# Kernel tuning notes

Measured on AMD Instinct MI355X. Metric: run time of the kernel, lower is better.

Reference implementation:

```python
import jax, jax.numpy as jnp
import numpy as np
from jax import lax

KSIZE = 33          # spatially-varying kernel is 33x33
PAD = 16            # ReplicationPad2d(16)
THRESH = 0.0001     # taps with weight <= 1e-4 are skipped (treated as zero)


def setup_inputs() -> dict:
    key = jax.random.key(0)
    k1, k2 = jax.random.split(key)
    inputImg = jax.random.uniform(k1, (1, 3, 256, 256), dtype=jnp.float32)
    Kernels = jax.random.uniform(k2, (1, KSIZE * KSIZE, 256, 256), dtype=jnp.float32)
    return {"inputImg": inputImg, "Kernels": Kernels}


def reference(inputImg, Kernels):
    B, C, H, W = inputImg.shape
    # Replication (edge) padding by 16 on both spatial dims
    padded = jnp.pad(inputImg, ((0, 0), (0, 0), (PAD, PAD), (PAD, PAD)), mode="edge")
    # Extract all 33x33 patches: [B, C*1089, H, W], channel-major then (fh, fw)
    patches = lax.conv_general_dilated_patches(
        padded, (KSIZE, KSIZE), (1, 1), "VALID",
        dimension_numbers=("NCHW", "OIHW", "NCHW"))
    patches = patches.reshape(B, C, KSIZE * KSIZE, H, W)
    # Threshold: original loop skips taps with kernel weight <= 1e-4
    Keff = jnp.where(Kernels > THRESH, Kernels, jnp.zeros_like(Kernels))  # [B, 1089, H, W]
    # Per-pixel dynamic convolution: sum over the 1089 taps
    out = jnp.einsum("bckhw,bkhw->bchw", patches, Keff)
    return out
```

## Files before the change

kernel.cpp:

```cpp
#include <hip/hip_runtime.h>

#define IMG_H 256
#define IMG_W 256
#define IMG_C 3
#define KS 33
#define PAD 16
#define THRESH 1e-4f
#define FH_PER 3

__global__ __launch_bounds__(256, 4)
void reblur_kernel(const float* __restrict__ img,
                   const float* __restrict__ ker,
                   float* __restrict__ out)
{
    const int x = threadIdx.x;
    const int y = blockIdx.x;
    const int chunk = blockIdx.y;
    const int fh0 = chunk * FH_PER;

    const int pix = y * IMG_W + x;
    const int plane = IMG_H * IMG_W;

    const float* kp = ker + (size_t)(fh0 * KS) * plane + pix;

    float a0 = 0.f, a1 = 0.f, a2 = 0.f;
    const int xm = x - PAD;

    #pragma unroll
    for (int dfh = 0; dfh < FH_PER; ++dfh) {
        int yy = y + (fh0 + dfh) - PAD;
        yy = yy < 0 ? 0 : (yy > IMG_H - 1 ? IMG_H - 1 : yy);
        const float* __restrict__ r0 = img + yy * IMG_W;
        const float* __restrict__ r1 = r0 + plane;
        const float* __restrict__ r2 = r1 + plane;
        #pragma unroll
        for (int fw = 0; fw < KS; ++fw) {
            float w = *kp;
            kp += plane;
            int xx = xm + fw;
            xx = xx < 0 ? 0 : (xx > IMG_W - 1 ? IMG_W - 1 : xx);
            float we = (w > THRESH) ? w : 0.f;
            a0 = fmaf(we, r0[xx], a0);
            a1 = fmaf(we, r1[xx], a1);
            a2 = fmaf(we, r2[xx], a2);
        }
    }

    atomicAdd(out + pix,             a0);
    atomicAdd(out + plane + pix,     a1);
    atomicAdd(out + 2 * plane + pix, a2);
}

extern "C" void kernel_launch(void* const* d_in, const int* in_sizes, int n_in,
                              void* d_out, int out_size, void* d_ws, size_t ws_size,
                              hipStream_t stream) {
    const float* img = (const float*)d_in[0];
    const float* ker = (const float*)d_in[1];
    float* out = (float*)d_out;

    hipMemsetAsync(out, 0, (size_t)out_size * sizeof(float), stream);

    dim3 grid(IMG_H, (KS + FH_PER - 1) / FH_PER);
    reblur_kernel<<<grid, IMG_W, 0, stream>>>(img, ker, out);
}
```

Baseline: 381.7 us.

## Stage padded image rows in LDS and compute four pixels per thread with float4

```diff
diff --git a/kernel.cpp b/kernel.cpp
--- a/kernel.cpp
+++ b/kernel.cpp
@@ -2,53 +2,116 @@
 
 #define IMG_H 256
 #define IMG_W 256
-#define IMG_C 3
 #define KS 33
 #define PAD 16
 #define THRESH 1e-4f
 #define FH_PER 3
+#define NCHUNK 11
+#define ROWS 4
+#define RSTG (ROWS + FH_PER - 1)
+#define LW (IMG_W + 2 * PAD)
+#define PLANE (IMG_H * IMG_W)
+
+__device__ __forceinline__ float f4c(const float4 v, int i) {
+    return i == 0 ? v.x : i == 1 ? v.y : i == 2 ? v.z : v.w;
+}
 
 __global__ __launch_bounds__(256, 4)
 void reblur_kernel(const float* __restrict__ img,
                    const float* __restrict__ ker,
                    float* __restrict__ out)
 {
-    const int x = threadIdx.x;
-    const int y = blockIdx.x;
-    const int chunk = blockIdx.y;
-    const int fh0 = chunk * FH_PER;
+    const int tid   = threadIdx.x;
+    const int wvid  = tid >> 6;
+    const int lane  = tid & 63;
+    const int ybase = blockIdx.x * ROWS;
+    const int y     = ybase + wvid;
+    const int fh0   = blockIdx.y * FH_PER;
+    const int x0    = lane * 4;
 
-    const int pix = y * IMG_W + x;
-    const int plane = IMG_H * IMG_W;
+    __shared__ __align__(16) float simg[3][RSTG][LW];
 
-    const float* kp = ker + (size_t)(fh0 * KS) * plane + pix;
+    const int tot = 3 * RSTG * LW;
+    for (int i = tid; i < tot; i += 256) {
+        const int c  = i / (RSTG * LW);
+        const int rm = i - c * (RSTG * LW);
+        const int r  = rm / LW;
+        const int px = rm - r * LW;
+        int yy = ybase + fh0 + r - PAD;
+        yy = yy < 0 ? 0 : (yy > IMG_H - 1 ? IMG_H - 1 : yy);
+        int xx = px - PAD;
+        xx = xx < 0 ? 0 : (xx > IMG_W - 1 ? IMG_W - 1 : xx);
+        simg[c][r][px] = img[c * PLANE + yy * IMG_W + xx];
+    }
+    __syncthreads();
 
-    float a0 = 0.f, a1 = 0.f, a2 = 0.f;
-    const int xm = x - PAD;
+    float acc[3][4] = {};
+
+    const float4* kb = reinterpret_cast<const float4*>(ker)
+                     + (size_t)fh0 * KS * (PLANE / 4) + y * (IMG_W / 4) + lane;
 
     #pragma unroll
     for (int dfh = 0; dfh < FH_PER; ++dfh) {
-        int yy = y + (fh0 + dfh) - PAD;
-        yy = yy < 0 ? 0 : (yy > IMG_H - 1 ? IMG_H - 1 : yy);
-        const float* __restrict__ r0 = img + yy * IMG_W;
-        const float* __restrict__ r1 = r0 + plane;
-        const float* __restrict__ r2 = r1 + plane;
+        const int r = wvid + dfh;
+        const float4* s0 = reinterpret_cast<const float4*>(&simg[0][r][x0]);
+        const float4* s1 = reinterpret_cast<const float4*>(&simg[1][r][x0]);
+        const float4* s2 = reinterpret_cast<const float4*>(&simg[2][r][x0]);
+        const float4* kf = kb + (size_t)(dfh * KS) * (PLANE / 4);
+
+        float4 a0 = s0[0], a1 = s1[0], a2 = s2[0];
+
         #pragma unroll
-        for (int fw = 0; fw < KS; ++fw) {
-            float w = *kp;
-            kp += plane;
-            int xx = xm + fw;
-            xx = xx < 0 ? 0 : (xx > IMG_W - 1 ? IMG_W - 1 : xx);
-            float we = (w > THRESH) ? w : 0.f;
-            a0 = fmaf(we, r0[xx], a0);
-            a1 = fmaf(we, r1[xx], a1);
-            a2 = fmaf(we, r2[xx], a2);
+        for (int g = 0; g < 8; ++g) {
+            const float4 b0 = s0[g + 1];
+            const float4 b1 = s1[g + 1];
+            const float4 b2 = s2[g + 1];
+            #pragma unroll
+            for (int j = 0; j < 4; ++j) {
+                const float4 wt = kf[(size_t)(4 * g + j) * (PLANE / 4)];
+                float4 th;
+                th.x = wt.x > THRESH ? wt.x : 0.f;
+                th.y = wt.y > THRESH ? wt.y : 0.f;
+                th.z = wt.z > THRESH ? wt.z : 0.f;
+                th.w = wt.w > THRESH ? wt.w : 0.f;
+                #pragma unroll
+                for (int p = 0; p < 4; ++p) {
+                    const int e = j + p;
+                    const float v0 = e < 4 ? f4c(a0, e) : f4c(b0, e - 4);
+                    const float v1 = e < 4 ? f4c(a1, e) : f4c(b1, e - 4);
+                    const float v2 = e < 4 ? f4c(a2, e) : f4c(b2, e - 4);
+                    const float w  = f4c(th, p);
+                    acc[0][p] = fmaf(w, v0, acc[0][p]);
+                    acc[1][p] = fmaf(w, v1, acc[1][p]);
+                    acc[2][p] = fmaf(w, v2, acc[2][p]);
+                }
+            }
+            a0 = b0; a1 = b1; a2 = b2;
+        }
+
+        {
+            const float4 wt = kf[(size_t)32 * (PLANE / 4)];
+            float4 th;
+            th.x = wt.x > THRESH ? wt.x : 0.f;
+            th.y = wt.y > THRESH ? wt.y : 0.f;
+            th.z = wt.z > THRESH ? wt.z : 0.f;
+            th.w = wt.w > THRESH ? wt.w : 0.f;
+            #pragma unroll
+            for (int p = 0; p < 4; ++p) {
+                const float w = f4c(th, p);
+                acc[0][p] = fmaf(w, f4c(a0, p), acc[0][p]);
+                acc[1][p] = fmaf(w, f4c(a1, p), acc[1][p]);
+                acc[2][p] = fmaf(w, f4c(a2, p), acc[2][p]);
+            }
         }
     }
 
-    atomicAdd(out + pix,             a0);
-    atomicAdd(out + plane + pix,     a1);
-    atomicAdd(out + 2 * plane + pix, a2);
+    const int obase = y * IMG_W + x0;
+    #pragma unroll
+    for (int p = 0; p < 4; ++p) {
+        atomicAdd(out + obase + p,             acc[0][p]);
+        atomicAdd(out + PLANE + obase + p,     acc[1][p]);
+        atomicAdd(out + 2 * PLANE + obase + p, acc[2][p]);
+    }
 }
 
 extern "C" void kernel_launch(void* const* d_in, const int* in_sizes, int n_in,
@@ -60,6 +123,6 @@
 
     hipMemsetAsync(out, 0, (size_t)out_size * sizeof(float), stream);
 
-    dim3 grid(IMG_H, (KS + FH_PER - 1) / FH_PER);
-    reblur_kernel<<<grid, IMG_W, 0, stream>>>(img, ker, out);
+    dim3 grid(IMG_H / ROWS, NCHUNK);
+    reblur_kernel<<<grid, 256, 0, stream>>>(img, ker, out);
 }
```

After: 415.7 us. 8.9% more time.
